# Kernel optimization log

Measured on AMD Instinct MI355X. Metric: run time of the kernel, lower is better.

The kernel has to match this reference:

```python
import jax, jax.numpy as jnp
import numpy as np

FEATURE_SIZE = 1_000_000
CROSS_EMB = 16
NNZ = 819_200
BATCH = 16_384
NEG_SAMPLING_RATE = 1.0


def setup_inputs() -> dict:
    key = jax.random.key(0)
    k_ids, k_seg, k_lw, k_cw, k_b = jax.random.split(key, 5)
    ids = jax.random.randint(k_ids, (NNZ,), 0, FEATURE_SIZE, dtype=jnp.int64 if jax.config.jax_enable_x64 else jnp.int32).astype(jnp.int32)
    segment_ids = jnp.sort(jax.random.randint(k_seg, (NNZ,), 0, BATCH, dtype=jnp.int32))
    linear_bias = jax.random.normal(k_b, (1,), dtype=jnp.float32) * 1e-4
    linear_w = jax.random.normal(k_lw, (FEATURE_SIZE, 1), dtype=jnp.float32) * 1e-4
    cross_emb_w = jax.random.normal(k_cw, (FEATURE_SIZE, CROSS_EMB), dtype=jnp.float32) * 1e-4
    return {
        "ids": ids,
        "segment_ids": segment_ids,
        "batch_size": BATCH,
        "linear_bias": linear_bias,
        "linear_w": linear_w,
        "cross_emb_w": cross_emb_w,
    }


def reference(ids, segment_ids, batch_size, linear_bias, linear_w, cross_emb_w):
    # Embedding-bag (sum combiner) == segment_sum of gathered rows.
    # Partitioned-shard routing in the original is mathematically a single
    # global gather + segment_sum (shard partial sums add up to the same).
    lin_rows = linear_w[ids]                        # [N, 1]
    logits_wide = jax.ops.segment_sum(lin_rows, segment_ids, num_segments=batch_size)  # [B, 1]
    logits_linear = linear_bias + logits_wide

    cross_rows = cross_emb_w[ids]                   # [N, D]
    summed = jax.ops.segment_sum(cross_rows, segment_ids, num_segments=batch_size)     # [B, D]
    squared_summed = jnp.square(summed)
    summed_squared = jax.ops.segment_sum(jnp.square(cross_rows), segment_ids, num_segments=batch_size)
    # FM second-order interaction term
    logits_cross = 0.5 * jnp.sum(squared_summed - summed_squared, axis=1, keepdims=True)  # [B, 1]

    logits = logits_linear + logits_cross
    logits_adjusted = logits + jnp.log(jnp.float32(NEG_SAMPLING_RATE))
    probabilities = jax.nn.sigmoid(logits_adjusted)
    return (logits, logits_adjusted, probabilities)
```

## Files before the change

### kernel.cpp

```cpp
#include <hip/hip_runtime.h>
#include <math.h>


__global__ __launch_bounds__(256) void fm_fused_kernel(
    const int* __restrict__ ids,
    const int* __restrict__ segs,
    const float* __restrict__ bias,
    const float* __restrict__ lw,
    const float* __restrict__ cw,
    float* __restrict__ out,
    int nnz, int batch)
{
    const int wave = threadIdx.x >> 6;
    const int wl   = threadIdx.x & 63;
    const int b    = blockIdx.x * 4 + wave;
    if (b >= batch) return;

    int target = b + (wl >> 5);
    int lo = 0, hi = nnz;
    while (lo < hi) {
        int mid = (lo + hi) >> 1;
        if (segs[mid] < target) lo = mid + 1; else hi = mid;
    }
    const int start = __shfl(lo, 0);
    const int end   = __shfl(lo, 32);

    const int e = wl >> 2;
    const int c = wl & 3;

    float4 sd = make_float4(0.f, 0.f, 0.f, 0.f);
    float ssq  = 0.f;
    float slin = 0.f;

    for (int i = start + e; i < end; i += 16) {
        const int id = ids[i];
        const float4 x = *reinterpret_cast<const float4*>(cw + ((size_t)id << 4) + (c << 2));
        sd.x += x.x; sd.y += x.y; sd.z += x.z; sd.w += x.w;
        ssq = fmaf(x.x, x.x, ssq);
        ssq = fmaf(x.y, x.y, ssq);
        ssq = fmaf(x.z, x.z, ssq);
        ssq = fmaf(x.w, x.w, ssq);
        if (c == 0) slin += lw[id];
    }

    #pragma unroll
    for (int m = 4; m <= 32; m <<= 1) {
        sd.x += __shfl_xor(sd.x, m);
        sd.y += __shfl_xor(sd.y, m);
        sd.z += __shfl_xor(sd.z, m);
        sd.w += __shfl_xor(sd.w, m);
        ssq  += __shfl_xor(ssq,  m);
        slin += __shfl_xor(slin, m);
    }
    float q = sd.x*sd.x + sd.y*sd.y + sd.z*sd.z + sd.w*sd.w;
    #pragma unroll
    for (int m = 1; m <= 2; m <<= 1) {
        q    += __shfl_xor(q,    m);
        ssq  += __shfl_xor(ssq,  m);
        slin += __shfl_xor(slin, m);
    }

    if (wl == 0) {
        const float logit = bias[0] + slin + 0.5f * (q - ssq);
        const float adj   = logit;
        out[b]             = logit;
        out[batch + b]     = adj;
        out[2 * batch + b] = 1.0f / (1.0f + expf(-adj));
    }
}

extern "C" void kernel_launch(void* const* d_in, const int* in_sizes, int n_in,
                              void* d_out, int out_size, void* d_ws, size_t ws_size,
                              hipStream_t stream) {
    const int*   ids  = (const int*)d_in[0];
    const int*   segs = (const int*)d_in[1];
    const float* bias = (const float*)d_in[3];
    const float* lw   = (const float*)d_in[4];
    const float* cw   = (const float*)d_in[5];
    float*       out  = (float*)d_out;

    const int nnz   = in_sizes[0];
    const int batch = out_size / 3;

    const int waves_per_block = 4;
    const int grid = (batch + waves_per_block - 1) / waves_per_block;
    fm_fused_kernel<<<grid, 256, 0, stream>>>(ids, segs, bias, lw, cw, out, nnz, batch);
}
```

Baseline: 135.7 us.

## Precompute segment offsets in a separate kernel and give each lane a whole row

Adds a pre-pass kernel that writes each segment's start offset into the workspace by detecting boundaries in the sorted segment ids. This replaces the per-wave binary search over the segment array. The main kernel now has each lane load an entire 16-float row (four float4 loads) instead of a quarter row, and reduces 16 accumulators across the wave with shuffles. This raises register pressure and shuffle count, and adds a second kernel launch plus extra traffic to write the offsets array.

```diff
diff --git a/kernel.cpp b/kernel.cpp
--- a/kernel.cpp
+++ b/kernel.cpp
@@ -2,65 +2,80 @@
 #include <math.h>
 
 
+__global__ __launch_bounds__(256) void seg_starts_kernel(
+    const int* __restrict__ segs, int* __restrict__ starts, int nnz, int batch)
+{
+    const int i = blockIdx.x * blockDim.x + threadIdx.x;
+    if (i >= nnz) return;
+    const int cur = segs[i];
+    if (i == 0) {
+        for (int b = 0; b <= cur; ++b) starts[b] = 0;
+    } else {
+        const int prev = segs[i - 1];
+        for (int b = prev + 1; b <= cur; ++b) starts[b] = i;
+    }
+    if (i == nnz - 1) {
+        for (int b = cur + 1; b <= batch; ++b) starts[b] = nnz;
+    }
+}
+
 __global__ __launch_bounds__(256) void fm_fused_kernel(
     const int* __restrict__ ids,
-    const int* __restrict__ segs,
+    const int* __restrict__ starts,
     const float* __restrict__ bias,
     const float* __restrict__ lw,
     const float* __restrict__ cw,
     float* __restrict__ out,
-    int nnz, int batch)
+    int batch)
 {
     const int wave = threadIdx.x >> 6;
     const int wl   = threadIdx.x & 63;
     const int b    = blockIdx.x * 4 + wave;
     if (b >= batch) return;
 
-    int target = b + (wl >> 5);
-    int lo = 0, hi = nnz;
-    while (lo < hi) {
-        int mid = (lo + hi) >> 1;
-        if (segs[mid] < target) lo = mid + 1; else hi = mid;
-    }
-    const int start = __shfl(lo, 0);
-    const int end   = __shfl(lo, 32);
+    const int start = starts[b];
+    const int end   = starts[b + 1];
 
-    const int e = wl >> 2;
-    const int c = wl & 3;
-
-    float4 sd = make_float4(0.f, 0.f, 0.f, 0.f);
-    float ssq  = 0.f;
+    float sd[16];
+    #pragma unroll
+    for (int d = 0; d < 16; ++d) sd[d] = 0.f;
+    float ssq = 0.f;
     float slin = 0.f;
 
-    for (int i = start + e; i < end; i += 16) {
+    for (int i = start + wl; i < end; i += 64) {
         const int id = ids[i];
-        const float4 x = *reinterpret_cast<const float4*>(cw + ((size_t)id << 4) + (c << 2));
-        sd.x += x.x; sd.y += x.y; sd.z += x.z; sd.w += x.w;
-        ssq = fmaf(x.x, x.x, ssq);
-        ssq = fmaf(x.y, x.y, ssq);
-        ssq = fmaf(x.z, x.z, ssq);
-        ssq = fmaf(x.w, x.w, ssq);
-        if (c == 0) slin += lw[id];
+        const float* row = cw + ((size_t)id << 4);
+        const float4 x0 = *reinterpret_cast<const float4*>(row);
+        const float4 x1 = *reinterpret_cast<const float4*>(row + 4);
+        const float4 x2 = *reinterpret_cast<const float4*>(row + 8);
+        const float4 x3 = *reinterpret_cast<const float4*>(row + 12);
+        slin += lw[id];
+        sd[ 0] += x0.x; sd[ 1] += x0.y; sd[ 2] += x0.z; sd[ 3] += x0.w;
+        sd[ 4] += x1.x; sd[ 5] += x1.y; sd[ 6] += x1.z; sd[ 7] += x1.w;
+        sd[ 8] += x2.x; sd[ 9] += x2.y; sd[10] += x2.z; sd[11] += x2.w;
+        sd[12] += x3.x; sd[13] += x3.y; sd[14] += x3.z; sd[15] += x3.w;
+        ssq = fmaf(x0.x, x0.x, ssq); ssq = fmaf(x0.y, x0.y, ssq);
+        ssq = fmaf(x0.z, x0.z, ssq); ssq = fmaf(x0.w, x0.w, ssq);
+        ssq = fmaf(x1.x, x1.x, ssq); ssq = fmaf(x1.y, x1.y, ssq);
+        ssq = fmaf(x1.z, x1.z, ssq); ssq = fmaf(x1.w, x1.w, ssq);
+        ssq = fmaf(x2.x, x2.x, ssq); ssq = fmaf(x2.y, x2.y, ssq);
+        ssq = fmaf(x2.z, x2.z, ssq); ssq = fmaf(x2.w, x2.w, ssq);
+        ssq = fmaf(x3.x, x3.x, ssq); ssq = fmaf(x3.y, x3.y, ssq);
+        ssq = fmaf(x3.w, x3.w, ssq); ssq = fmaf(x3.z, x3.z, ssq);
     }
 
     #pragma unroll
-    for (int m = 4; m <= 32; m <<= 1) {
-        sd.x += __shfl_xor(sd.x, m);
-        sd.y += __shfl_xor(sd.y, m);
-        sd.z += __shfl_xor(sd.z, m);
-        sd.w += __shfl_xor(sd.w, m);
-        ssq  += __shfl_xor(ssq,  m);
-        slin += __shfl_xor(slin, m);
-    }
-    float q = sd.x*sd.x + sd.y*sd.y + sd.z*sd.z + sd.w*sd.w;
-    #pragma unroll
-    for (int m = 1; m <= 2; m <<= 1) {
-        q    += __shfl_xor(q,    m);
+    for (int m = 1; m < 64; m <<= 1) {
+        #pragma unroll
+        for (int d = 0; d < 16; ++d) sd[d] += __shfl_xor(sd[d], m);
         ssq  += __shfl_xor(ssq,  m);
         slin += __shfl_xor(slin, m);
     }
 
     if (wl == 0) {
+        float q = 0.f;
+        #pragma unroll
+        for (int d = 0; d < 16; ++d) q = fmaf(sd[d], sd[d], q);
         const float logit = bias[0] + slin + 0.5f * (q - ssq);
         const float adj   = logit;
         out[b]             = logit;
@@ -82,7 +97,11 @@
     const int nnz   = in_sizes[0];
     const int batch = out_size / 3;
 
+    int* starts = (int*)d_ws;
+
+    seg_starts_kernel<<<(nnz + 255) / 256, 256, 0, stream>>>(segs, starts, nnz, batch);
+
     const int waves_per_block = 4;
     const int grid = (batch + waves_per_block - 1) / waves_per_block;
-    fm_fused_kernel<<<grid, 256, 0, stream>>>(ids, segs, bias, lw, cw, out, nnz, batch);
+    fm_fused_kernel<<<grid, 256, 0, stream>>>(ids, starts, bias, lw, cw, out, batch);
 }
```

Result: faster. 125.0 us (-7.9%).
